# Optimization experiments

Hardware: AMD Instinct MI355X
Metric: run time of the kernel (lower is better)

Reference implementation:

```python
import jax, jax.numpy as jnp
import numpy as np
from jax import lax
from jax.scipy.special import logsumexp

B, T, K = 256, 1024, 64


def setup_inputs() -> dict:
    key = jax.random.key(0)
    k1, k2, k3 = jax.random.split(key, 3)
    y_true = jax.random.randint(k1, (B, T), 0, K)  # 0 == pad tag
    emissions = jax.random.normal(k2, (B, T, K), dtype=jnp.float32)
    transition = jax.random.normal(k3, (K, K), dtype=jnp.float32) * 0.1
    return {"y_true": y_true, "emissions": emissions, "transition": transition}


def _log_partition(emissions, mask, transition):
    # alpha_0 = emissions[:, 0, :] (TF code does not mask step 0)
    alpha0 = emissions[:, 0, :]  # [B, K]

    def step(alpha, xs):
        emit_t, m_t = xs  # [B, K], [B]
        # score[b, i, j] = alpha[b, i] + transition[i, j] + emit_t[b, j]
        score = alpha[:, :, None] + transition[None, :, :] + emit_t[:, None, :]
        new_a = logsumexp(score, axis=1)  # [B, K]
        new_a = jnp.where(m_t[:, None] > 0, new_a, alpha)
        return new_a, None

    xs = (jnp.swapaxes(emissions[:, 1:, :], 0, 1),  # [T-1, B, K]
          jnp.swapaxes(mask[:, 1:], 0, 1))           # [T-1, B]
    alpha, _ = lax.scan(step, alpha0, xs)
    return logsumexp(alpha, axis=1)  # [B]


def reference(y_true, emissions, transition):
    mask = (y_true != 0).astype(emissions.dtype)  # [B, T]
    yt = y_true.astype(jnp.int32)

    # emission scores of the gold path on masked emissions
    em_masked = emissions * mask[:, :, None]
    e_scores = jnp.take_along_axis(em_masked, yt[:, :, None], axis=2)[..., 0].sum(axis=1)  # [B]

    # transition scores of the gold path
    prev, nxt = yt[:, :-1], yt[:, 1:]
    t_scores = (transition[prev, nxt] * mask[:, 1:]).sum(axis=1)  # [B]

    log_z = _log_partition(emissions, mask, transition)  # [B]
    ll = e_scores + t_scores - log_z
    return -jnp.mean(ll)
```

## Files before the change

### kernel.cpp

```cpp
#include <hip/hip_runtime.h>

#define LOG2E 1.44269504088896340736f
#define LN2   0.69314718055994530942f

typedef short bf8 __attribute__((ext_vector_type(8)));
typedef float f4  __attribute__((ext_vector_type(4)));

static __device__ __forceinline__ unsigned short f2bf_rne(float f) {
    unsigned u = __float_as_uint(f);
    u += 0x7FFFu + ((u >> 16) & 1u);
    return (unsigned short)(u >> 16);
}
static __device__ __forceinline__ unsigned pack_bf_trunc(float lo, float hi) {
    return __builtin_amdgcn_perm(__float_as_uint(hi), __float_as_uint(lo), 0x07060302u);
}

__global__ __attribute__((amdgpu_flat_work_group_size(64, 64), amdgpu_waves_per_eu(2, 4)))
void crf_scan(const int* __restrict__ yg, const float* __restrict__ em,
              const float* __restrict__ tr, unsigned short* __restrict__ Pg)
{
    constexpr int T = 1024;
    const int c = blockIdx.x, b = blockIdx.y;
    const int lane = threadIdx.x, nl = lane & 15, q = lane >> 4;

    __shared__ __align__(16) float d_sh[64];

    bf8 afr[4][2];
    #pragma unroll
    for (int mt = 0; mt < 4; ++mt) {
        const int g = 32 * (mt >> 1) + 8 * (nl >> 2) + 4 * (mt & 1) + (nl & 3);
        #pragma unroll
        for (int ka = 0; ka < 2; ++ka) {
            bf8 v;
            #pragma unroll
            for (int j = 0; j < 8; ++j) {
                const int k = 32 * ka + 8 * q + j;
                v[j] = (short)f2bf_rne(exp2f(tr[k * 64 + g] * LOG2E));
            }
            afr[mt][ka] = v;
        }
    }

    bf8 bfr[2][4];
    #pragma unroll
    for (int kt = 0; kt < 2; ++kt)
        #pragma unroll
        for (int nt = 0; nt < 4; ++nt) {
            bf8 v;
            #pragma unroll
            for (int j = 0; j < 8; ++j)
                v[j] = (short)((32 * kt + 8 * q + j == 16 * nt + nl) ? 0x3F80 : 0);
            bfr[kt][nt] = v;
        }

    const int t0 = 1 + 64 * c;
    const int nsteps = (c == 15) ? 63 : 64;
    const float* emb = em + (size_t)b * T * 64;

    int tl = t0 + lane; if (tl > T - 1) tl = T - 1;
    const int yvl = yg[b * T + tl];
    const unsigned long long msk = __ballot(lane < nsteps && yvl != 0);

    float ldc = emb[t0 * 64 + lane];
    for (int s = 0; s < nsteps; ++s) {
        int tn = t0 + s + 1; if (tn > T - 1) tn = T - 1;
        const float ldn = emb[tn * 64 + lane];
        if ((msk >> s) & 1ull) {
            d_sh[lane] = exp2f(ldc * LOG2E - 7.0f);
            f4 dq[4];
            #pragma unroll
            for (int mt = 0; mt < 4; ++mt)
                dq[mt] = *(const f4*)&d_sh[32 * (mt >> 1) + 4 * (mt & 1) + 8 * q];
            #pragma unroll
            for (int nt = 0; nt < 4; ++nt) {
                f4 acc[4];
                #pragma unroll
                for (int mt = 0; mt < 4; ++mt) {
                    f4 a = __builtin_amdgcn_mfma_f32_16x16x32_bf16(
                               afr[mt][0], bfr[0][nt], (f4)(0.0f), 0, 0, 0);
                    acc[mt] = __builtin_amdgcn_mfma_f32_16x16x32_bf16(
                               afr[mt][1], bfr[1][nt], a, 0, 0, 0);
                }
                #pragma unroll
                for (int kt = 0; kt < 2; ++kt) {
                    union { uint4 u; bf8 v8; } wv;
                    wv.u.x = pack_bf_trunc(acc[2*kt  ][0] * dq[2*kt  ][0],
                                           acc[2*kt  ][1] * dq[2*kt  ][1]);
                    wv.u.y = pack_bf_trunc(acc[2*kt  ][2] * dq[2*kt  ][2],
                                           acc[2*kt  ][3] * dq[2*kt  ][3]);
                    wv.u.z = pack_bf_trunc(acc[2*kt+1][0] * dq[2*kt+1][0],
                                           acc[2*kt+1][1] * dq[2*kt+1][1]);
                    wv.u.w = pack_bf_trunc(acc[2*kt+1][2] * dq[2*kt+1][2],
                                           acc[2*kt+1][3] * dq[2*kt+1][3]);
                    bfr[kt][nt] = wv.v8;
                }
            }
        }
        ldc = ldn;
    }

    unsigned short* pg = Pg + ((size_t)(b * 16 + c) << 12);
    #pragma unroll
    for (int nt = 0; nt < 4; ++nt)
        #pragma unroll
        for (int kt = 0; kt < 2; ++kt)
            *(uint4*)(pg + (16 * nt + nl) * 64 + 32 * kt + 8 * q) =
                *(const uint4*)&bfr[kt][nt];
}

__global__ __attribute__((amdgpu_flat_work_group_size(256, 256)))
void crf_combine(const int* __restrict__ yg, const float* __restrict__ em,
                 const float* __restrict__ tr, const unsigned short* __restrict__ Pg,
                 float* __restrict__ out)
{
    constexpr int T = 1024;
    const int b = blockIdx.x, tid = threadIdx.x;
    const int w = tid >> 6, j = tid & 63;

    __shared__ __align__(16) float v_sh[64];
    __shared__ float red[3][4];

    float ep = 0.f, tp = 0.f; int cnt = 0;
    float v = 0.f, L = 0.f, vs = 0.f;

    if (w == 0) {
        const float e0 = em[(size_t)b * T * 64 + j];
        float M0 = e0;
        #pragma unroll
        for (int o = 32; o > 0; o >>= 1) M0 = fmaxf(M0, __shfl_xor(M0, o, 64));
        v = exp2f((e0 - M0) * LOG2E);
        L = M0;

        const unsigned short* row = Pg + ((size_t)(b * 16) << 12) + j * 64;
        uint4 pA[8], pB[8];
        #pragma unroll
        for (int r = 0; r < 8; ++r) pA[r] = *(const uint4*)(row + r * 8);

#define CHUNK_STEP(CUR, NXT, CIDX)                                                 \
        do {                                                                       \
            if ((CIDX) + 1 < 16) {      \
                const unsigned short* rn = row + ((size_t)((CIDX) + 1) << 12);     \
                _Pragma("unroll")                                                  \
                for (int r = 0; r < 8; ++r) NXT[r] = *(const uint4*)(rn + r * 8);  \
            }                                                                      \
            v_sh[j] = v;                             \
            float s0 = 0.f, s1 = 0.f, s2 = 0.f, s3 = 0.f;                          \
            _Pragma("unroll")                                                      \
            for (int r = 0; r < 8; ++r) {                                          \
                const uint4 qq = CUR[r];                                           \
                const float* vp = &v_sh[r * 8];                                    \
                s0 = fmaf(__uint_as_float(qq.x << 16),         vp[0], s0);         \
                s1 = fmaf(__uint_as_float(qq.x & 0xFFFF0000u), vp[1], s1);         \
                s2 = fmaf(__uint_as_float(qq.y << 16),         vp[2], s2);         \
                s3 = fmaf(__uint_as_float(qq.y & 0xFFFF0000u), vp[3], s3);         \
                s0 = fmaf(__uint_as_float(qq.z << 16),         vp[4], s0);         \
                s1 = fmaf(__uint_as_float(qq.z & 0xFFFF0000u), vp[5], s1);         \
                s2 = fmaf(__uint_as_float(qq.w << 16),         vp[6], s2);         \
                s3 = fmaf(__uint_as_float(qq.w & 0xFFFF0000u), vp[7], s3);         \
            }                                                                      \
            float s = (s0 + s1) + (s2 + s3);                                       \
            const unsigned sb =                                                    \
                (unsigned)__builtin_amdgcn_readlane((int)__float_as_uint(s), 0);   \
            const int ef = (int)((sb >> 23) & 0xFF);                               \
            if (ef > 0 && ef < 255 && ef != 127) {       \
                const int E = ef - 127;                                            \
                s *= __uint_as_float((unsigned)(127 - E) << 23);                   \
                L += (float)E * LN2;                                               \
            }                                                                      \
            v = s;                                                                 \
        } while (0)

        for (int cc = 0; cc < 16; cc += 2) {
            CHUNK_STEP(pA, pB, cc);
            CHUNK_STEP(pB, pA, cc + 1);
        }
#undef CHUNK_STEP

        vs = v;
        #pragma unroll
        for (int o = 32; o > 0; o >>= 1) vs += __shfl_xor(vs, o, 64);
    } else {
        const int* yb = yg + b * T;
        const int wt = tid - 64;
        for (int t = 1 + wt; t < T; t += 192) {
            const int yt = yb[t];
            if (yt != 0) {
                ++cnt;
                tp += tr[yb[t - 1] * 64 + yt];
                ep += em[((size_t)b * T + t) * 64 + yt];
            }
        }
        if (tid == 64) {
            const int y0 = yb[0];
            if (y0 != 0) ep += em[(size_t)b * T * 64 + y0];
        }
        #pragma unroll
        for (int o = 32; o > 0; o >>= 1) {
            ep  += __shfl_xor(ep, o, 64);
            tp  += __shfl_xor(tp, o, 64);
            cnt += __shfl_xor(cnt, o, 64);
        }
        if (j == 0) { red[0][w] = ep; red[1][w] = tp; red[2][w] = (float)cnt; }
    }
    __syncthreads();

    if (tid == 0) {
        const float eps = red[0][1] + red[0][2] + red[0][3];
        const float tps = red[1][1] + red[1][2] + red[1][3];
        const float cs  = red[2][1] + red[2][2] + red[2][3];
        const float logz = L + 7.0f * LN2 * cs + __log2f(vs) * LN2;
        atomicAdd(out, (eps + tps - logz) * (-1.0f / 256.0f));
    }
}

extern "C" void kernel_launch(void* const* d_in, const int* in_sizes, int n_in,
                              void* d_out, int out_size, void* d_ws, size_t ws_size,
                              hipStream_t stream) {
    const int*   y  = (const int*)d_in[0];
    const float* em = (const float*)d_in[1];
    const float* tr = (const float*)d_in[2];
    float* out = (float*)d_out;
    unsigned short* Pg = (unsigned short*)d_ws;

    hipMemsetAsync(out, 0, sizeof(float), stream);
    crf_scan<<<dim3(16, 256), dim3(64), 0, stream>>>(y, em, tr, Pg);
    crf_combine<<<dim3(256), dim3(256), 0, stream>>>(y, em, tr, Pg, out);
}
```

Baseline: 203.4 us.

## Split scan chunk's 4 column tiles across 4 waves per block

The chunked scan kernel now launches 256 threads per block, and each wave owns one 16-column tile of the 64x64 running product instead of one wave handling all four tiles. This cuts the serial MFMA dependency chain per wave by four and spreads the work of each step over more waves, aiming to shorten the latency-bound per-step loop. In exchange, every wave redundantly loads the transition fragments and recomputes the emission scaling, and the total wave count rises fourfold.

```diff
diff --git a/kernel.cpp b/kernel.cpp
--- a/kernel.cpp
+++ b/kernel.cpp
@@ -15,15 +15,17 @@
     return __builtin_amdgcn_perm(__float_as_uint(hi), __float_as_uint(lo), 0x07060302u);
 }
 
-__global__ __attribute__((amdgpu_flat_work_group_size(64, 64), amdgpu_waves_per_eu(2, 4)))
+__global__ __attribute__((amdgpu_flat_work_group_size(256, 256), amdgpu_waves_per_eu(4)))
 void crf_scan(const int* __restrict__ yg, const float* __restrict__ em,
               const float* __restrict__ tr, unsigned short* __restrict__ Pg)
 {
     constexpr int T = 1024;
     const int c = blockIdx.x, b = blockIdx.y;
-    const int lane = threadIdx.x, nl = lane & 15, q = lane >> 4;
-
-    __shared__ __align__(16) float d_sh[64];
+    const int tid = threadIdx.x;
+    const int w = tid >> 6;
+    const int lane = tid & 63, nl = lane & 15, q = lane >> 4;
+
+    __shared__ __align__(16) float d_sh[4][64];
 
     bf8 afr[4][2];
     #pragma unroll
@@ -41,17 +43,15 @@
         }
     }
 
-    bf8 bfr[2][4];
+    bf8 bfr[2];
     #pragma unroll
-    for (int kt = 0; kt < 2; ++kt)
-        #pragma unroll
-        for (int nt = 0; nt < 4; ++nt) {
-            bf8 v;
-            #pragma unroll
-            for (int j = 0; j < 8; ++j)
-                v[j] = (short)((32 * kt + 8 * q + j == 16 * nt + nl) ? 0x3F80 : 0);
-            bfr[kt][nt] = v;
-        }
+    for (int kt = 0; kt < 2; ++kt) {
+        bf8 v;
+        #pragma unroll
+        for (int j = 0; j < 8; ++j)
+            v[j] = (short)((32 * kt + 8 * q + j == 16 * w + nl) ? 0x3F80 : 0);
+        bfr[kt] = v;
+    }
 
     const int t0 = 1 + 64 * c;
     const int nsteps = (c == 15) ? 63 : 64;
@@ -66,34 +66,31 @@
         int tn = t0 + s + 1; if (tn > T - 1) tn = T - 1;
         const float ldn = emb[tn * 64 + lane];
         if ((msk >> s) & 1ull) {
-            d_sh[lane] = exp2f(ldc * LOG2E - 7.0f);
+            d_sh[w][lane] = exp2f(ldc * LOG2E - 7.0f);
             f4 dq[4];
             #pragma unroll
             for (int mt = 0; mt < 4; ++mt)
-                dq[mt] = *(const f4*)&d_sh[32 * (mt >> 1) + 4 * (mt & 1) + 8 * q];
-            #pragma unroll
-            for (int nt = 0; nt < 4; ++nt) {
-                f4 acc[4];
-                #pragma unroll
-                for (int mt = 0; mt < 4; ++mt) {
-                    f4 a = __builtin_amdgcn_mfma_f32_16x16x32_bf16(
-                               afr[mt][0], bfr[0][nt], (f4)(0.0f), 0, 0, 0);
-                    acc[mt] = __builtin_amdgcn_mfma_f32_16x16x32_bf16(
-                               afr[mt][1], bfr[1][nt], a, 0, 0, 0);
-                }
-                #pragma unroll
-                for (int kt = 0; kt < 2; ++kt) {
-                    union { uint4 u; bf8 v8; } wv;
-                    wv.u.x = pack_bf_trunc(acc[2*kt  ][0] * dq[2*kt  ][0],
-                                           acc[2*kt  ][1] * dq[2*kt  ][1]);
-                    wv.u.y = pack_bf_trunc(acc[2*kt  ][2] * dq[2*kt  ][2],
-                                           acc[2*kt  ][3] * dq[2*kt  ][3]);
-                    wv.u.z = pack_bf_trunc(acc[2*kt+1][0] * dq[2*kt+1][0],
-                                           acc[2*kt+1][1] * dq[2*kt+1][1]);
-                    wv.u.w = pack_bf_trunc(acc[2*kt+1][2] * dq[2*kt+1][2],
-                                           acc[2*kt+1][3] * dq[2*kt+1][3]);
-                    bfr[kt][nt] = wv.v8;
-                }
+                dq[mt] = *(const f4*)&d_sh[w][32 * (mt >> 1) + 4 * (mt & 1) + 8 * q];
+            f4 acc[4];
+            #pragma unroll
+            for (int mt = 0; mt < 4; ++mt) {
+                f4 a = __builtin_amdgcn_mfma_f32_16x16x32_bf16(
+                           afr[mt][0], bfr[0], (f4)(0.0f), 0, 0, 0);
+                acc[mt] = __builtin_amdgcn_mfma_f32_16x16x32_bf16(
+                           afr[mt][1], bfr[1], a, 0, 0, 0);
+            }
+            #pragma unroll
+            for (int kt = 0; kt < 2; ++kt) {
+                union { uint4 u; bf8 v8; } wv;
+                wv.u.x = pack_bf_trunc(acc[2*kt  ][0] * dq[2*kt  ][0],
+                                       acc[2*kt  ][1] * dq[2*kt  ][1]);
+                wv.u.y = pack_bf_trunc(acc[2*kt  ][2] * dq[2*kt  ][2],
+                                       acc[2*kt  ][3] * dq[2*kt  ][3]);
+                wv.u.z = pack_bf_trunc(acc[2*kt+1][0] * dq[2*kt+1][0],
+                                       acc[2*kt+1][1] * dq[2*kt+1][1]);
+                wv.u.w = pack_bf_trunc(acc[2*kt+1][2] * dq[2*kt+1][2],
+                                       acc[2*kt+1][3] * dq[2*kt+1][3]);
+                bfr[kt] = wv.v8;
             }
         }
         ldc = ldn;
@@ -101,11 +98,9 @@
 
     unsigned short* pg = Pg + ((size_t)(b * 16 + c) << 12);
     #pragma unroll
-    for (int nt = 0; nt < 4; ++nt)
-        #pragma unroll
-        for (int kt = 0; kt < 2; ++kt)
-            *(uint4*)(pg + (16 * nt + nl) * 64 + 32 * kt + 8 * q) =
-                *(const uint4*)&bfr[kt][nt];
+    for (int kt = 0; kt < 2; ++kt)
+        *(uint4*)(pg + (16 * w + nl) * 64 + 32 * kt + 8 * q) =
+            *(const uint4*)&bfr[kt];
 }
 
 __global__ __attribute__((amdgpu_flat_work_group_size(256, 256)))
@@ -223,6 +218,6 @@
     unsigned short* Pg = (unsigned short*)d_ws;
 
     hipMemsetAsync(out, 0, sizeof(float), stream);
-    crf_scan<<<dim3(16, 256), dim3(64), 0, stream>>>(y, em, tr, Pg);
+    crf_scan<<<dim3(16, 256), dim3(256), 0, stream>>>(y, em, tr, Pg);
     crf_combine<<<dim3(256), dim3(256), 0, stream>>>(y, em, tr, Pg, out);
 }
```

New measurement: 245.1 us. 1.21x slower.

## Software-pipeline MFMA bursts with packing across column groups in CRF scan

Applied to the files above, without the earlier changes.

The per-step loop of the scan kernel is restructured so that the MFMA products for one column group are issued while the previous group's results are scaled and packed to bf16. The next step's first group is started early, and sched_barriers keep the interleaved order. The masked-step branch becomes a branchless select on the packed results, so inactive steps now do the full matmul work. MFMAs are issued through volatile inline asm and the launch bounds change, which takes hazard handling and scheduling freedom away from the compiler.

```diff
diff --git a/kernel.cpp b/kernel.cpp
--- a/kernel.cpp
+++ b/kernel.cpp
@@ -5,6 +5,7 @@
 
 typedef short bf8 __attribute__((ext_vector_type(8)));
 typedef float f4  __attribute__((ext_vector_type(4)));
+typedef float f2  __attribute__((ext_vector_type(2)));
 
 static __device__ __forceinline__ unsigned short f2bf_rne(float f) {
     unsigned u = __float_as_uint(f);
@@ -15,7 +16,15 @@
     return __builtin_amdgcn_perm(__float_as_uint(hi), __float_as_uint(lo), 0x07060302u);
 }
 
-__global__ __attribute__((amdgpu_flat_work_group_size(64, 64), amdgpu_waves_per_eu(2, 4)))
+static __device__ __forceinline__ f4 mfma_v(bf8 a, bf8 b, f4 c) {
+    f4 d;
+    asm volatile("v_mfma_f32_16x16x32_bf16 %0, %1, %2, %3"
+                 : "=v"(d) : "v"(a), "v"(b), "v"(c));
+    return d;
+}
+#define SB() __builtin_amdgcn_sched_barrier(0)
+
+__global__ __launch_bounds__(64, 2)
 void crf_scan(const int* __restrict__ yg, const float* __restrict__ em,
               const float* __restrict__ tr, unsigned short* __restrict__ Pg)
 {
@@ -53,51 +62,80 @@
             bfr[kt][nt] = v;
         }
 
+    const f4 zc = (f4)(0.0f);
+
     const int t0 = 1 + 64 * c;
     const int nsteps = (c == 15) ? 63 : 64;
     const float* emb = em + (size_t)b * T * 64;
 
     int tl = t0 + lane; if (tl > T - 1) tl = T - 1;
-    const int yvl = yg[b * T + tl];
-    const unsigned long long msk = __ballot(lane < nsteps && yvl != 0);
+    const unsigned long long msk = __ballot(lane < nsteps && yg[b * T + tl] != 0);
+
+#define BURST(ACC, G)                                                        \
+    { _Pragma("unroll")                                                      \
+      for (int mt = 0; mt < 4; ++mt) {                                       \
+          f4 t4 = mfma_v(afr[mt][0], bfr[0][G], zc);                         \
+          ACC[mt] = mfma_v(afr[mt][1], bfr[1][G], t4);                       \
+      } }
+
+#define PACK(ACC, G, ACT)                                                    \
+    { _Pragma("unroll")                                                      \
+      for (int kt = 0; kt < 2; ++kt) {                                       \
+          f2 a0, a1, b0, b1;                                                 \
+          a0[0] = ACC[2*kt  ][0]; a0[1] = ACC[2*kt  ][1];                    \
+          a1[0] = ACC[2*kt  ][2]; a1[1] = ACC[2*kt  ][3];                    \
+          b0[0] = ACC[2*kt+1][0]; b0[1] = ACC[2*kt+1][1];                    \
+          b1[0] = ACC[2*kt+1][2]; b1[1] = ACC[2*kt+1][3];                    \
+          a0 *= dp[2*kt  ][0];  a1 *= dp[2*kt  ][1];       \
+          b0 *= dp[2*kt+1][0];  b1 *= dp[2*kt+1][1];                         \
+          union { uint4 uu; bf8 v8; } wv, od;                                \
+          od.v8 = bfr[kt][G];                                                \
+          const unsigned nx = pack_bf_trunc(a0[0], a0[1]);                   \
+          const unsigned ny = pack_bf_trunc(a1[0], a1[1]);                   \
+          const unsigned nz = pack_bf_trunc(b0[0], b0[1]);                   \
+          const unsigned nw = pack_bf_trunc(b1[0], b1[1]);                   \
+          wv.uu.x = (ACT) ? nx : od.uu.x;                                    \
+          wv.uu.y = (ACT) ? ny : od.uu.y;                                    \
+          wv.uu.z = (ACT) ? nz : od.uu.z;                                    \
+          wv.uu.w = (ACT) ? nw : od.uu.w;                                    \
+          bfr[kt][G] = wv.v8;                                                \
+      } }
+
+#define LOAD_DP()                                                            \
+    { _Pragma("unroll")                                                      \
+      for (int mt = 0; mt < 4; ++mt) {                                       \
+          const float* dsrc = &d_sh[32 * (mt >> 1) + 4 * (mt & 1) + 8 * q];  \
+          dp[mt][0] = *(const f2*)&dsrc[0];                                  \
+          dp[mt][1] = *(const f2*)&dsrc[2];                                  \
+      } }
 
     float ldc = emb[t0 * 64 + lane];
+    d_sh[lane] = exp2f(ldc * LOG2E - 7.0f);
+    f2 dp[4][2];
+    LOAD_DP();
+    f4 aA[4], aB[4];
+    BURST(aA, 0);
+
     for (int s = 0; s < nsteps; ++s) {
         int tn = t0 + s + 1; if (tn > T - 1) tn = T - 1;
         const float ldn = emb[tn * 64 + lane];
-        if ((msk >> s) & 1ull) {
-            d_sh[lane] = exp2f(ldc * LOG2E - 7.0f);
-            f4 dq[4];
-            #pragma unroll
-            for (int mt = 0; mt < 4; ++mt)
-                dq[mt] = *(const f4*)&d_sh[32 * (mt >> 1) + 4 * (mt & 1) + 8 * q];
-            #pragma unroll
-            for (int nt = 0; nt < 4; ++nt) {
-                f4 acc[4];
-                #pragma unroll
-                for (int mt = 0; mt < 4; ++mt) {
-                    f4 a = __builtin_amdgcn_mfma_f32_16x16x32_bf16(
-                               afr[mt][0], bfr[0][nt], (f4)(0.0f), 0, 0, 0);
-                    acc[mt] = __builtin_amdgcn_mfma_f32_16x16x32_bf16(
-                               afr[mt][1], bfr[1][nt], a, 0, 0, 0);
-                }
-                #pragma unroll
-                for (int kt = 0; kt < 2; ++kt) {
-                    union { uint4 u; bf8 v8; } wv;
-                    wv.u.x = pack_bf_trunc(acc[2*kt  ][0] * dq[2*kt  ][0],
-                                           acc[2*kt  ][1] * dq[2*kt  ][1]);
-                    wv.u.y = pack_bf_trunc(acc[2*kt  ][2] * dq[2*kt  ][2],
-                                           acc[2*kt  ][3] * dq[2*kt  ][3]);
-                    wv.u.z = pack_bf_trunc(acc[2*kt+1][0] * dq[2*kt+1][0],
-                                           acc[2*kt+1][1] * dq[2*kt+1][1]);
-                    wv.u.w = pack_bf_trunc(acc[2*kt+1][2] * dq[2*kt+1][2],
-                                           acc[2*kt+1][3] * dq[2*kt+1][3]);
-                    bfr[kt][nt] = wv.v8;
-                }
-            }
-        }
+        const bool act = (msk >> s) & 1ull;
+        SB(); BURST(aB, 1);
+        SB(); PACK(aA, 0, act);
+        SB(); BURST(aA, 2);
+        SB(); PACK(aB, 1, act);
+        SB(); BURST(aB, 3);
+        SB(); PACK(aA, 2, act);
+        SB(); BURST(aA, 0);
+        SB(); PACK(aB, 3, act);
+        SB();
         ldc = ldn;
-    }
+        d_sh[lane] = exp2f(ldc * LOG2E - 7.0f);
+        LOAD_DP();
+    }
+#undef BURST
+#undef PACK
+#undef LOAD_DP
 
     unsigned short* pg = Pg + ((size_t)(b * 16 + c) << 12);
     #pragma unroll
```

Result: slower. 216.1 us (+6.2%).

## Pack four scan waves per block, use packed f32 multiplies and MFMA priority

Applied to the files above, without the earlier changes.

Regroups the chunked scan so each 256-thread block runs four independent 64-lane waves (one time chunk each), with per-wave shared scratch, replacing 4096 single-wave blocks with 1024 larger ones. The scaling multiply is rewritten on float2 vectors so the compiler can emit packed FP32 multiplies, and s_setprio raises wave priority around the MFMA burst. The goal is better packing of waves per CU and cheaper elementwise work. The trade-off is that the waves_per_eu hint is dropped, which could change register allocation.

```diff
diff --git a/kernel.cpp b/kernel.cpp
--- a/kernel.cpp
+++ b/kernel.cpp
@@ -5,6 +5,7 @@
 
 typedef short bf8 __attribute__((ext_vector_type(8)));
 typedef float f4  __attribute__((ext_vector_type(4)));
+typedef float f2  __attribute__((ext_vector_type(2)));
 
 static __device__ __forceinline__ unsigned short f2bf_rne(float f) {
     unsigned u = __float_as_uint(f);
@@ -15,15 +16,17 @@
     return __builtin_amdgcn_perm(__float_as_uint(hi), __float_as_uint(lo), 0x07060302u);
 }
 
-__global__ __attribute__((amdgpu_flat_work_group_size(64, 64), amdgpu_waves_per_eu(2, 4)))
+__global__ __attribute__((amdgpu_flat_work_group_size(256, 256)))
 void crf_scan(const int* __restrict__ yg, const float* __restrict__ em,
               const float* __restrict__ tr, unsigned short* __restrict__ Pg)
 {
     constexpr int T = 1024;
-    const int c = blockIdx.x, b = blockIdx.y;
-    const int lane = threadIdx.x, nl = lane & 15, q = lane >> 4;
-
-    __shared__ __align__(16) float d_sh[64];
+    const int b = blockIdx.y;
+    const int wv = threadIdx.x >> 6;
+    const int c = blockIdx.x * 4 + wv;
+    const int lane = threadIdx.x & 63, nl = lane & 15, q = lane >> 4;
+
+    __shared__ __align__(16) float d_sh[4][64];
 
     bf8 afr[4][2];
     #pragma unroll
@@ -66,14 +69,18 @@
         int tn = t0 + s + 1; if (tn > T - 1) tn = T - 1;
         const float ldn = emb[tn * 64 + lane];
         if ((msk >> s) & 1ull) {
-            d_sh[lane] = exp2f(ldc * LOG2E - 7.0f);
-            f4 dq[4];
-            #pragma unroll
-            for (int mt = 0; mt < 4; ++mt)
-                dq[mt] = *(const f4*)&d_sh[32 * (mt >> 1) + 4 * (mt & 1) + 8 * q];
+            d_sh[wv][lane] = exp2f(ldc * LOG2E - 7.0f);
+            f2 dp[4][2];
+            #pragma unroll
+            for (int mt = 0; mt < 4; ++mt) {
+                const float* dsrc = &d_sh[wv][32 * (mt >> 1) + 4 * (mt & 1) + 8 * q];
+                dp[mt][0] = *(const f2*)&dsrc[0];
+                dp[mt][1] = *(const f2*)&dsrc[2];
+            }
             #pragma unroll
             for (int nt = 0; nt < 4; ++nt) {
                 f4 acc[4];
+                __builtin_amdgcn_s_setprio(1);
                 #pragma unroll
                 for (int mt = 0; mt < 4; ++mt) {
                     f4 a = __builtin_amdgcn_mfma_f32_16x16x32_bf16(
@@ -81,18 +88,22 @@
                     acc[mt] = __builtin_amdgcn_mfma_f32_16x16x32_bf16(
                                afr[mt][1], bfr[1][nt], a, 0, 0, 0);
                 }
+                __builtin_amdgcn_s_setprio(0);
                 #pragma unroll
                 for (int kt = 0; kt < 2; ++kt) {
-                    union { uint4 u; bf8 v8; } wv;
-                    wv.u.x = pack_bf_trunc(acc[2*kt  ][0] * dq[2*kt  ][0],
-                                           acc[2*kt  ][1] * dq[2*kt  ][1]);
-                    wv.u.y = pack_bf_trunc(acc[2*kt  ][2] * dq[2*kt  ][2],
-                                           acc[2*kt  ][3] * dq[2*kt  ][3]);
-                    wv.u.z = pack_bf_trunc(acc[2*kt+1][0] * dq[2*kt+1][0],
-                                           acc[2*kt+1][1] * dq[2*kt+1][1]);
-                    wv.u.w = pack_bf_trunc(acc[2*kt+1][2] * dq[2*kt+1][2],
-                                           acc[2*kt+1][3] * dq[2*kt+1][3]);
-                    bfr[kt][nt] = wv.v8;
+                    f2 a0, a1, b0, b1;
+                    a0[0] = acc[2*kt  ][0]; a0[1] = acc[2*kt  ][1];
+                    a1[0] = acc[2*kt  ][2]; a1[1] = acc[2*kt  ][3];
+                    b0[0] = acc[2*kt+1][0]; b0[1] = acc[2*kt+1][1];
+                    b1[0] = acc[2*kt+1][2]; b1[1] = acc[2*kt+1][3];
+                    a0 *= dp[2*kt  ][0];  a1 *= dp[2*kt  ][1];
+                    b0 *= dp[2*kt+1][0];  b1 *= dp[2*kt+1][1];
+                    union { uint4 uu; bf8 v8; } wvv;
+                    wvv.uu.x = pack_bf_trunc(a0[0], a0[1]);
+                    wvv.uu.y = pack_bf_trunc(a1[0], a1[1]);
+                    wvv.uu.z = pack_bf_trunc(b0[0], b0[1]);
+                    wvv.uu.w = pack_bf_trunc(b1[0], b1[1]);
+                    bfr[kt][nt] = wvv.v8;
                 }
             }
         }
@@ -223,6 +234,6 @@
     unsigned short* Pg = (unsigned short*)d_ws;
 
     hipMemsetAsync(out, 0, sizeof(float), stream);
-    crf_scan<<<dim3(16, 256), dim3(64), 0, stream>>>(y, em, tr, Pg);
+    crf_scan<<<dim3(4, 256), dim3(256), 0, stream>>>(y, em, tr, Pg);
     crf_combine<<<dim3(256), dim3(256), 0, stream>>>(y, em, tr, Pg, out);
 }
```

New measurement: 226.8 us. +11.5%, slower.
